# Optimization experiments

Hardware: AMD Instinct MI355X
Metric: run time of the kernel (lower is better)

The kernel has to match this reference:

```python
import jax, jax.numpy as jnp
import numpy as np

NUM_HEADS = 4
EPS = 1e-5


def setup_inputs() -> dict:
    key = jax.random.key(0)
    ks = jax.random.split(key, 5)
    B, C, H, W = 1, 128, 64, 64
    x = jax.random.normal(ks[0], (B, C, H, W), dtype=jnp.float32)
    # 1x1 conv weights [out_c, in_c]; scaled ~ kaiming-ish to keep softmax non-degenerate
    s = 1.0 / np.sqrt(C)
    qw = jax.random.normal(ks[1], (C, C), dtype=jnp.float32) * s
    kw = jax.random.normal(ks[2], (C, C), dtype=jnp.float32) * s
    vw = jax.random.normal(ks[3], (C, C), dtype=jnp.float32) * s
    pw = jax.random.normal(ks[4], (C, C), dtype=jnp.float32) * s
    zeros = jnp.zeros((C,), dtype=jnp.float32)
    return {
        "x": x,
        "gn_w": jnp.ones((C,), dtype=jnp.float32),
        "gn_b": zeros,
        "qw": qw, "qb": zeros,
        "kw": kw, "kb": zeros,
        "vw": vw, "vb": zeros,
        "pw": pw, "pb": zeros,
    }


def reference(x, gn_w, gn_b, qw, qb, kw, kb, vw, vb, pw, pb):
    B, C, H, W = x.shape
    N = H * W
    d = C // NUM_HEADS

    # GroupNorm(num_groups=1): normalize over (C,H,W) per sample, per-channel affine
    mean = jnp.mean(x, axis=(1, 2, 3), keepdims=True)
    var = jnp.var(x, axis=(1, 2, 3), keepdims=True)
    h = (x - mean) * jax.lax.rsqrt(var + EPS)
    h = h * gn_w[None, :, None, None] + gn_b[None, :, None, None]

    hf = h.reshape(B, C, N)  # [B,C,N]

    def conv1x1(w, b):  # 1x1 conv == channel GEMM
        return jnp.einsum('oc,bcn->bon', w, hf) + b[None, :, None]

    q = conv1x1(qw, qb).reshape(B, NUM_HEADS, d, N)
    k = conv1x1(kw, kb).reshape(B, NUM_HEADS, d, N)
    v = conv1x1(vw, vb).reshape(B, NUM_HEADS, d, N)

    scale = d ** (-0.5)
    attn = jnp.einsum('bhdn,bhdm->bhnm', q, k) * scale  # [B,H,N,N]
    attn = jax.nn.softmax(attn, axis=-1)
    out = jnp.einsum('bhnm,bhdm->bhdn', attn, v)  # [B,H,d,N]

    out = out.reshape(B, C, N)
    out = jnp.einsum('oc,bcn->bon', pw, out) + pb[None, :, None]
    return x + out.reshape(B, C, H, W)
```

## Files before the change

kernel.cpp:

```cpp
#include <hip/hip_runtime.h>

#define NPOS 4096
#define NCH  128
#define NTOT (NPOS * NCH)
#define NHEAD 4
#define DH    32
#define NSPLIT 4
#define KSPAN (NPOS / NSPLIT)
#define NTILE (KSPAN / 64)

typedef __attribute__((ext_vector_type(8))) short short8;
typedef __attribute__((ext_vector_type(4))) float floatx4;
typedef unsigned short u16;
typedef unsigned int   u32;

__device__ __forceinline__ u16 f2bf(float f) {
  u32 u = __float_as_uint(f);
  u += 0x7fffu + ((u >> 16) & 1u);
  return (u16)(u >> 16);
}
__device__ __forceinline__ u32 pack2bf(float a, float b) {
  return (u32)f2bf(a) | ((u32)f2bf(b) << 16);
}
__device__ __forceinline__ u32 pack2bf_fast(float a, float b) {
  return ((__float_as_uint(a) + 0x8000u) >> 16) |
         ((__float_as_uint(b) + 0x8000u) & 0xffff0000u);
}
__device__ __forceinline__ float bf2f(u16 h) {
  return __uint_as_float(((u32)h) << 16);
}

__global__ __launch_bounds__(256) void gn_prep_k(const float* __restrict__ x,
                                                 float2* __restrict__ partials,
                                                 u32* __restrict__ bounds,
                                                 const float* __restrict__ qw, const float* __restrict__ kw,
                                                 const float* __restrict__ vw, const float* __restrict__ pw,
                                                 u16* __restrict__ wq, u16* __restrict__ wk,
                                                 u16* __restrict__ wv, u16* __restrict__ wp) {
  int i = blockIdx.x * 256 + threadIdx.x;
  int w = threadIdx.x >> 6, lane = threadIdx.x & 63;
  float4 a = ((const float4*)x)[i];
  float s  = a.x + a.y + a.z + a.w;
  float sq = a.x*a.x + a.y*a.y + a.z*a.z + a.w*a.w;
#pragma unroll
  for (int m = 1; m < 64; m <<= 1) {
    s  += __shfl_xor(s, m);
    sq += __shfl_xor(sq, m);
  }
  __shared__ float red[8];
  if (lane == 0) { red[w] = s; red[4 + w] = sq; }
  __syncthreads();
  if (threadIdx.x == 0)
    partials[blockIdx.x] = make_float2(red[0]+red[1]+red[2]+red[3],
                                       red[4]+red[5]+red[6]+red[7]);
  if (blockIdx.x == 0 && threadIdx.x < 4) bounds[threadIdx.x] = 0;
  if (blockIdx.x < 16) {
    int t = blockIdx.x * 256 + threadIdx.x;
    const float sc = 0.17677669529663687f * 1.4426950408889634f;
    float4 v = ((const float4*)qw)[t];
    ((uint2*)wq)[t] = make_uint2(pack2bf(v.x*sc, v.y*sc), pack2bf(v.z*sc, v.w*sc));
    v = ((const float4*)kw)[t];
    ((uint2*)wk)[t] = make_uint2(pack2bf(v.x, v.y), pack2bf(v.z, v.w));
    v = ((const float4*)vw)[t];
    ((uint2*)wv)[t] = make_uint2(pack2bf(v.x, v.y), pack2bf(v.z, v.w));
    v = ((const float4*)pw)[t];
    ((uint2*)wp)[t] = make_uint2(pack2bf(v.x, v.y), pack2bf(v.z, v.w));
  }
}

__global__ __launch_bounds__(768) void qkv_k(const float* __restrict__ x,
    const float* __restrict__ gw, const float* __restrict__ gb,
    const float2* __restrict__ partials,
    const u16* __restrict__ wq, const u16* __restrict__ wk, const u16* __restrict__ wv,
    const float* __restrict__ qb, const float* __restrict__ kb, const float* __restrict__ vb,
    u16* __restrict__ q, u16* __restrict__ k, u16* __restrict__ v, u32* __restrict__ bounds) {
  const int t = threadIdx.x;
  const int w = t >> 6, lane = t & 63;
  const int l16 = lane & 15, quad = lane >> 4;
  const int n0 = blockIdx.x * 16;
  const floatx4 zero = {0.f, 0.f, 0.f, 0.f};

  __shared__ float red[16];
  __shared__ float2 swb[128];
  __shared__ __align__(16) u16 hs[16][136];

  if (t < 512) {
    float2 p = partials[t];
    float s = p.x, sq = p.y;
#pragma unroll
    for (int m = 1; m < 64; m <<= 1) {
      s  += __shfl_xor(s, m);
      sq += __shfl_xor(sq, m);
    }
    if (lane == 0) { red[w] = s; red[8 + w] = sq; }
  }
  __syncthreads();
  float mean = (red[0]+red[1]+red[2]+red[3]+red[4]+red[5]+red[6]+red[7]) * (1.0f / NTOT);
  float var  = (red[8]+red[9]+red[10]+red[11]+red[12]+red[13]+red[14]+red[15]) * (1.0f / NTOT)
               - mean * mean;
  float rstd = rsqrtf(var + 1e-5f);
  if (t < 128) {
    float swv = gw[t] * rstd;
    swb[t] = make_float2(swv, gb[t] - mean * swv);
  }
  __syncthreads();
  if (t < 512) {
    int c = t >> 2, seg = t & 3;
    float4 xv = *(const float4*)(x + (size_t)c * NPOS + n0 + seg * 4);
    float2 sb = swb[c];
    int nl = seg * 4;
    hs[nl + 0][c] = f2bf(xv.x * sb.x + sb.y);
    hs[nl + 1][c] = f2bf(xv.y * sb.x + sb.y);
    hs[nl + 2][c] = f2bf(xv.z * sb.x + sb.y);
    hs[nl + 3][c] = f2bf(xv.w * sb.x + sb.y);
  }
  __syncthreads();

  short8 bfr[4];
#pragma unroll
  for (int kk = 0; kk < 4; kk++)
    bfr[kk] = *(const short8*)&hs[l16][kk * 32 + quad * 8];

  const int mat = w >> 2, head = w & 3, ow = head * 32;
  const u16* wm = (mat == 0) ? wq : (mat == 1) ? wk : wv;
  floatx4 a0 = zero, a1 = zero;
  const u16* ap = wm + (size_t)(ow + l16) * NCH + quad * 8;
#pragma unroll
  for (int kk = 0; kk < 4; kk++) {
    a0 = __builtin_amdgcn_mfma_f32_16x16x32_bf16(*(const short8*)(ap + kk*32),          bfr[kk], a0, 0,0,0);
    a1 = __builtin_amdgcn_mfma_f32_16x16x32_bf16(*(const short8*)(ap + 16*NCH + kk*32), bfr[kk], a1, 0,0,0);
  }
  const int n = n0 + l16;
  if (mat == 0) {
    const float sc = 0.17677669529663687f * 1.4426950408889634f;
    u16* qp = q + (size_t)(head * NPOS + n) * DH;
#pragma unroll
    for (int ss = 0; ss < 2; ss++) {
      floatx4 acc = ss ? a1 : a0;
      int od = ss * 16 + quad * 4;
      float r0 = acc[0] + qb[ow+od+0]*sc, r1 = acc[1] + qb[ow+od+1]*sc;
      float r2 = acc[2] + qb[ow+od+2]*sc, r3 = acc[3] + qb[ow+od+3]*sc;
      *(uint2*)(qp + od) = make_uint2(pack2bf(r0, r1), pack2bf(r2, r3));
    }
  } else if (mat == 1) {
    float sumsq = 0.f;
    u16* kp = k + (size_t)(head * NPOS + n) * DH;
#pragma unroll
    for (int ss = 0; ss < 2; ss++) {
      floatx4 acc = ss ? a1 : a0;
      int od = ss * 16 + quad * 4;
      float r0 = acc[0] + kb[ow+od+0], r1 = acc[1] + kb[ow+od+1];
      float r2 = acc[2] + kb[ow+od+2], r3 = acc[3] + kb[ow+od+3];
      sumsq += r0*r0 + r1*r1 + r2*r2 + r3*r3;
      *(uint2*)(kp + od) = make_uint2(pack2bf(r0, r1), pack2bf(r2, r3));
    }
    sumsq += __shfl_xor(sumsq, 16);
    sumsq += __shfl_xor(sumsq, 32);
#pragma unroll
    for (int m = 1; m < 16; m <<= 1) sumsq = fmaxf(sumsq, __shfl_xor(sumsq, m));
    if (lane == 0) atomicMax(&bounds[head], __float_as_uint(sumsq));
  } else {
    u16* vp = v + (size_t)(head * DH) * NPOS + n;
#pragma unroll
    for (int ss = 0; ss < 2; ss++) {
      floatx4 acc = ss ? a1 : a0;
      int od = ss * 16 + quad * 4;
#pragma unroll
      for (int r = 0; r < 4; r++)
        vp[(size_t)(od + r) * NPOS] = f2bf(acc[r] + vb[ow + od + r]);
    }
  }
}

__global__ __launch_bounds__(256) void attn_k(const u16* __restrict__ q, const u16* __restrict__ k,
                                              const u16* __restrict__ v, const u32* __restrict__ bounds,
                                              u32* __restrict__ Opair, float* __restrict__ lpart) {
  const int w = threadIdx.x >> 6, lane = threadIdx.x & 63;
  const int l16 = lane & 15, quad = lane >> 4;
  const int s = blockIdx.x >> 8;
  const int q0 = (blockIdx.x & 255) * 16;
  const int head = w;
  __shared__ __align__(16) u16 p_lds[4][2][16][72];

  short8 bq = *(const short8*)(q + (size_t)(head * NPOS + q0 + l16) * DH + quad * 8);
  float qn2 = 0.f;
#pragma unroll
  for (int j = 0; j < 8; j++) { float f = bf2f((u16)bq[j]); qn2 += f * f; }
  qn2 += __shfl_xor(qn2, 16);
  qn2 += __shfl_xor(qn2, 32);
  float kmax = sqrtf(__uint_as_float(bounds[head])) * 1.0005f;
  float bound = sqrtf(qn2) * kmax;

  floatx4 o0 = {0,0,0,0}, o1 = {0,0,0,0}, ol = {0,0,0,0};
  short8 ones;
#pragma unroll
  for (int j = 0; j < 8; j++) ones[j] = (short)0x3F80;

  const u16* kbp = k + (size_t)head * NPOS * DH + quad * 8;
  const u16* vb0 = v + (size_t)(head * DH + l16) * NPOS + quad * 8;
  const u16* vb1 = vb0 + (size_t)16 * NPOS;
  const floatx4 zero = {0,0,0,0};

  int m0 = s * KSPAN;
  short8 ak[4], av[4];
#pragma unroll
  for (int sub = 0; sub < 4; sub++)
    ak[sub] = *(const short8*)(kbp + (size_t)(m0 + sub * 16 + l16) * DH);
#pragma unroll
  for (int kc = 0; kc < 2; kc++) {
    av[2*kc]   = *(const short8*)(vb0 + m0 + kc * 32);
    av[2*kc+1] = *(const short8*)(vb1 + m0 + kc * 32);
  }

  for (int it = 0; it < NTILE; it++) {
    const int mn = m0 + 64;
    const bool more = (it + 1 < NTILE);
    short8 nak[4], nav[4];
    if (more) {
#pragma unroll
      for (int sub = 0; sub < 4; sub++)
        nak[sub] = *(const short8*)(kbp + (size_t)(mn + sub * 16 + l16) * DH);
#pragma unroll
      for (int kc = 0; kc < 2; kc++) {
        nav[2*kc]   = *(const short8*)(vb0 + mn + kc * 32);
        nav[2*kc+1] = *(const short8*)(vb1 + mn + kc * 32);
      }
    }
    const int buf = it & 1;
    floatx4 c[4];
#pragma unroll
    for (int sub = 0; sub < 4; sub++)
      c[sub] = __builtin_amdgcn_mfma_f32_16x16x32_bf16(ak[sub], bq, zero, 0, 0, 0);
#pragma unroll
    for (int sub = 0; sub < 4; sub++) {
      float p0 = __builtin_amdgcn_exp2f(c[sub][0] - bound);
      float p1 = __builtin_amdgcn_exp2f(c[sub][1] - bound);
      float p2 = __builtin_amdgcn_exp2f(c[sub][2] - bound);
      float p3 = __builtin_amdgcn_exp2f(c[sub][3] - bound);
      *(uint2*)&p_lds[w][buf][l16][sub * 16 + quad * 4] =
          make_uint2(pack2bf_fast(p0, p1), pack2bf_fast(p2, p3));
    }
#pragma unroll
    for (int kc = 0; kc < 2; kc++) {
      short8 pa = *(const short8*)&p_lds[w][buf][l16][kc * 32 + quad * 8];
      o0 = __builtin_amdgcn_mfma_f32_16x16x32_bf16(pa, av[2*kc],   o0, 0, 0, 0);
      o1 = __builtin_amdgcn_mfma_f32_16x16x32_bf16(pa, av[2*kc+1], o1, 0, 0, 0);
      ol = __builtin_amdgcn_mfma_f32_16x16x32_bf16(pa, ones,       ol, 0, 0, 0);
    }
    if (more) {
#pragma unroll
      for (int j = 0; j < 4; j++) { ak[j] = nak[j]; av[j] = nav[j]; }
    }
    m0 = mn;
  }

  u32*   op = Opair + (size_t)(s * NHEAD + head) * NPOS * 16;
  float* lp = lpart + (size_t)(s * NHEAD + head) * NPOS;
#pragma unroll
  for (int r = 0; r < 4; r++) {
    int qq = q0 + quad * 4 + r;
    op[(size_t)qq * 16 + l16] = pack2bf(o0[r], o1[r]);
    if (l16 == 0) lp[qq] = ol[r];
  }
}

__global__ __launch_bounds__(512) void proj_k(const u32* __restrict__ Opair,
                                              const float* __restrict__ lpart,
                                              const u16* __restrict__ wp,
                                              const float* __restrict__ pb,
                                              const float* __restrict__ x,
                                              float* __restrict__ out) {
  const int t = threadIdx.x;
  const int w = t >> 6, lane = t & 63;
  const int l16 = lane & 15, quad = lane >> 4;
  const int n0 = blockIdx.x * 16;
  const floatx4 zero = {0.f, 0.f, 0.f, 0.f};
  __shared__ __align__(16) u16 at_lds[16][136];

  {
    const int n = t & 15, ci = t >> 4;
    const int c0 = ci * 4, head = c0 >> 5, off = c0 & 31;
    const int half = off >> 4, j0 = off & 15;
    float acc[4] = {0.f, 0.f, 0.f, 0.f};
    float l = 0.f;
#pragma unroll
    for (int s2 = 0; s2 < NSPLIT; s2++) {
      const u32* pp = Opair + ((size_t)(s2 * NHEAD + head) * NPOS + n0 + n) * 16 + j0;
      uint4 u = *(const uint4*)pp;
      u32 uu[4] = {u.x, u.y, u.z, u.w};
#pragma unroll
      for (int j = 0; j < 4; j++)
        acc[j] += half ? __uint_as_float(uu[j] & 0xffff0000u)
                       : __uint_as_float(uu[j] << 16);
      l += lpart[(size_t)(s2 * NHEAD + head) * NPOS + n0 + n];
    }
    float inv = 1.0f / fmaxf(l, 1e-30f);
    *(uint2*)&at_lds[n][c0] = make_uint2(pack2bf(acc[0]*inv, acc[1]*inv),
                                         pack2bf(acc[2]*inv, acc[3]*inv));
  }
  __syncthreads();

  short8 bfr[4];
#pragma unroll
  for (int kk = 0; kk < 4; kk++)
    bfr[kk] = *(const short8*)&at_lds[l16][kk * 32 + quad * 8];
  const int ow = w * 16;
  floatx4 a0 = zero;
  const u16* ap = wp + (size_t)(ow + l16) * NCH + quad * 8;
#pragma unroll
  for (int kk = 0; kk < 4; kk++)
    a0 = __builtin_amdgcn_mfma_f32_16x16x32_bf16(*(const short8*)(ap + kk*32), bfr[kk], a0, 0,0,0);
  const int n = n0 + l16;
#pragma unroll
  for (int r = 0; r < 4; r++) {
    int o = ow + quad * 4 + r;
    size_t idx = (size_t)o * NPOS + n;
    out[idx] = a0[r] + pb[o] + x[idx];
  }
}

extern "C" void kernel_launch(void* const* d_in, const int* in_sizes, int n_in,
                              void* d_out, int out_size, void* d_ws, size_t ws_size,
                              hipStream_t stream) {
  const float* x   = (const float*)d_in[0];
  const float* gnw = (const float*)d_in[1];
  const float* gnb = (const float*)d_in[2];
  const float* qw  = (const float*)d_in[3];
  const float* qb  = (const float*)d_in[4];
  const float* kw  = (const float*)d_in[5];
  const float* kb  = (const float*)d_in[6];
  const float* vw  = (const float*)d_in[7];
  const float* vb  = (const float*)d_in[8];
  const float* pw  = (const float*)d_in[9];
  const float* pb  = (const float*)d_in[10];
  float* out = (float*)d_out;

  char* wsb = (char*)d_ws;
  float2* partials = (float2*)wsb;
  u32*    bounds   = (u32*)(wsb + 4096);
  u16* wqb = (u16*)(wsb + 8192);
  u16* wkb = wqb + 16384;
  u16* wvb = wkb + 16384;
  u16* wpb = wvb + 16384;
  u16* qbuf = wpb + 16384;
  u16* kbuf = qbuf + NTOT;
  u16* vbuf = kbuf + NTOT;
  u32* Opair = (u32*)(vbuf + NTOT);
  float* lpart = (float*)(Opair + (size_t)NSPLIT * NHEAD * NPOS * 16);

  gn_prep_k<<<512, 256, 0, stream>>>(x, partials, bounds, qw, kw, vw, pw,
                                     wqb, wkb, wvb, wpb);
  qkv_k<<<256, 768, 0, stream>>>(x, gnw, gnb, partials, wqb, wkb, wvb,
                                 qb, kb, vb, qbuf, kbuf, vbuf, bounds);
  attn_k<<<256 * NSPLIT, 256, 0, stream>>>(qbuf, kbuf, vbuf, bounds, Opair, lpart);
  proj_k<<<256, 512, 0, stream>>>(Opair, lpart, wpb, pb, x, out);
}
```

Before: 144.5 us.

## Permute key rows so QK MFMA output feeds PV MFMA directly from registers

Reorders which key positions each lane loads for the QK^T MFMA so the accumulator layout matches the A-operand layout needed by the P·V MFMA. The probabilities are exponentiated and packed in registers instead of round-tripping through a shared-memory P buffer, which removes LDS stores, loads and the associated waits. Correctness relies on the permuted key index mapping staying consistent with the V columns consumed per k-chunk.

```diff
diff --git a/kernel.cpp b/kernel.cpp
--- a/kernel.cpp
+++ b/kernel.cpp
@@ -180,7 +180,6 @@
   const int s = blockIdx.x >> 8;
   const int q0 = (blockIdx.x & 255) * 16;
   const int head = w;
-  __shared__ __align__(16) u16 p_lds[4][2][16][72];
 
   short8 bq = *(const short8*)(q + (size_t)(head * NPOS + q0 + l16) * DH + quad * 8);
   float qn2 = 0.f;
@@ -196,6 +195,11 @@
 #pragma unroll
   for (int j = 0; j < 8; j++) ones[j] = (short)0x3F80;
 
+  int ko[4];
+#pragma unroll
+  for (int s2 = 0; s2 < 4; s2++)
+    ko[s2] = 32 * (s2 >> 1) + (l16 >> 2) * 8 + (s2 & 1) * 4 + (l16 & 3);
+
   const u16* kbp = k + (size_t)head * NPOS * DH + quad * 8;
   const u16* vb0 = v + (size_t)(head * DH + l16) * NPOS + quad * 8;
   const u16* vb1 = vb0 + (size_t)16 * NPOS;
@@ -204,8 +208,8 @@
   int m0 = s * KSPAN;
   short8 ak[4], av[4];
 #pragma unroll
-  for (int sub = 0; sub < 4; sub++)
-    ak[sub] = *(const short8*)(kbp + (size_t)(m0 + sub * 16 + l16) * DH);
+  for (int s2 = 0; s2 < 4; s2++)
+    ak[s2] = *(const short8*)(kbp + (size_t)(m0 + ko[s2]) * DH);
 #pragma unroll
   for (int kc = 0; kc < 2; kc++) {
     av[2*kc]   = *(const short8*)(vb0 + m0 + kc * 32);
@@ -218,31 +222,31 @@
     short8 nak[4], nav[4];
     if (more) {
 #pragma unroll
-      for (int sub = 0; sub < 4; sub++)
-        nak[sub] = *(const short8*)(kbp + (size_t)(mn + sub * 16 + l16) * DH);
+      for (int s2 = 0; s2 < 4; s2++)
+        nak[s2] = *(const short8*)(kbp + (size_t)(mn + ko[s2]) * DH);
 #pragma unroll
       for (int kc = 0; kc < 2; kc++) {
         nav[2*kc]   = *(const short8*)(vb0 + mn + kc * 32);
         nav[2*kc+1] = *(const short8*)(vb1 + mn + kc * 32);
       }
     }
-    const int buf = it & 1;
     floatx4 c[4];
 #pragma unroll
-    for (int sub = 0; sub < 4; sub++)
-      c[sub] = __builtin_amdgcn_mfma_f32_16x16x32_bf16(ak[sub], bq, zero, 0, 0, 0);
-#pragma unroll
-    for (int sub = 0; sub < 4; sub++) {
-      float p0 = __builtin_amdgcn_exp2f(c[sub][0] - bound);
-      float p1 = __builtin_amdgcn_exp2f(c[sub][1] - bound);
-      float p2 = __builtin_amdgcn_exp2f(c[sub][2] - bound);
-      float p3 = __builtin_amdgcn_exp2f(c[sub][3] - bound);
-      *(uint2*)&p_lds[w][buf][l16][sub * 16 + quad * 4] =
-          make_uint2(pack2bf_fast(p0, p1), pack2bf_fast(p2, p3));
-    }
+    for (int s2 = 0; s2 < 4; s2++)
+      c[s2] = __builtin_amdgcn_mfma_f32_16x16x32_bf16(ak[s2], bq, zero, 0, 0, 0);
 #pragma unroll
     for (int kc = 0; kc < 2; kc++) {
-      short8 pa = *(const short8*)&p_lds[w][buf][l16][kc * 32 + quad * 8];
+      float pa0 = __builtin_amdgcn_exp2f(c[2*kc][0] - bound);
+      float pa1 = __builtin_amdgcn_exp2f(c[2*kc][1] - bound);
+      float pa2 = __builtin_amdgcn_exp2f(c[2*kc][2] - bound);
+      float pa3 = __builtin_amdgcn_exp2f(c[2*kc][3] - bound);
+      float pb0 = __builtin_amdgcn_exp2f(c[2*kc+1][0] - bound);
+      float pb1 = __builtin_amdgcn_exp2f(c[2*kc+1][1] - bound);
+      float pb2 = __builtin_amdgcn_exp2f(c[2*kc+1][2] - bound);
+      float pb3 = __builtin_amdgcn_exp2f(c[2*kc+1][3] - bound);
+      uint4 uu = make_uint4(pack2bf_fast(pa0, pa1), pack2bf_fast(pa2, pa3),
+                            pack2bf_fast(pb0, pb1), pack2bf_fast(pb2, pb3));
+      short8 pa = *(short8*)&uu;
       o0 = __builtin_amdgcn_mfma_f32_16x16x32_bf16(pa, av[2*kc],   o0, 0, 0, 0);
       o1 = __builtin_amdgcn_mfma_f32_16x16x32_bf16(pa, av[2*kc+1], o1, 0, 0, 0);
       ol = __builtin_amdgcn_mfma_f32_16x16x32_bf16(pa, ones,       ol, 0, 0, 0);
```

Result: no change. 145.5 us (+0.7%).

## Register-block four query tiles per wave and drop the LDS round trip for P

Applied to the files above, without the earlier changes.

Each wave now processes 64 queries as four 16-row fragments, so every K/V fragment it loads feeds four times as many MFMAs. K rows are loaded in a permuted order so the QK^T MFMA output can be packed straight into the A operand of the PV MFMA, which removes the shared-memory store and reload of P. The softmax bound is folded into the MFMA accumulator init, the key range is split eight ways instead of four, and K/V loads are double-buffered in registers. The costs are higher register pressure (hinted with launch_bounds 256,2) and twice as many partial outputs for the projection kernel to combine.

```diff
diff --git a/kernel.cpp b/kernel.cpp
--- a/kernel.cpp
+++ b/kernel.cpp
@@ -5,7 +5,7 @@
 #define NTOT (NPOS * NCH)
 #define NHEAD 4
 #define DH    32
-#define NSPLIT 4
+#define NSPLIT 8
 #define KSPAN (NPOS / NSPLIT)
 #define NTILE (KSPAN / 64)
 
@@ -172,95 +172,117 @@
   }
 }
 
-__global__ __launch_bounds__(256) void attn_k(const u16* __restrict__ q, const u16* __restrict__ k,
-                                              const u16* __restrict__ v, const u32* __restrict__ bounds,
-                                              u32* __restrict__ Opair, float* __restrict__ lpart) {
+__global__ __launch_bounds__(256, 2) void attn_k(const u16* __restrict__ q, const u16* __restrict__ k,
+                                                 const u16* __restrict__ v, const u32* __restrict__ bounds,
+                                                 u32* __restrict__ Opair, float* __restrict__ lpart) {
   const int w = threadIdx.x >> 6, lane = threadIdx.x & 63;
   const int l16 = lane & 15, quad = lane >> 4;
-  const int s = blockIdx.x >> 8;
-  const int q0 = (blockIdx.x & 255) * 16;
+  const int s = blockIdx.x >> 6;
+  const int q0w = (blockIdx.x & 63) * 64;
   const int head = w;
-  __shared__ __align__(16) u16 p_lds[4][2][16][72];
-
-  short8 bq = *(const short8*)(q + (size_t)(head * NPOS + q0 + l16) * DH + quad * 8);
-  float qn2 = 0.f;
-#pragma unroll
-  for (int j = 0; j < 8; j++) { float f = bf2f((u16)bq[j]); qn2 += f * f; }
-  qn2 += __shfl_xor(qn2, 16);
-  qn2 += __shfl_xor(qn2, 32);
+
   float kmax = sqrtf(__uint_as_float(bounds[head])) * 1.0005f;
-  float bound = sqrtf(qn2) * kmax;
-
-  floatx4 o0 = {0,0,0,0}, o1 = {0,0,0,0}, ol = {0,0,0,0};
+
+  short8 bq[4];
+  floatx4 cb[4];
+#pragma unroll
+  for (int qf = 0; qf < 4; qf++) {
+    bq[qf] = *(const short8*)(q + (size_t)(head * NPOS + q0w + qf * 16 + l16) * DH + quad * 8);
+    float qn2 = 0.f;
+#pragma unroll
+    for (int j = 0; j < 8; j++) { float f = bf2f((u16)bq[qf][j]); qn2 += f * f; }
+    qn2 += __shfl_xor(qn2, 16);
+    qn2 += __shfl_xor(qn2, 32);
+    float nb = -sqrtf(qn2) * kmax;
+    cb[qf][0] = nb; cb[qf][1] = nb; cb[qf][2] = nb; cb[qf][3] = nb;
+  }
+
+  floatx4 o0[4], o1[4], ol[4];
+#pragma unroll
+  for (int qf = 0; qf < 4; qf++) {
+    o0[qf] = (floatx4){0,0,0,0}; o1[qf] = (floatx4){0,0,0,0}; ol[qf] = (floatx4){0,0,0,0};
+  }
   short8 ones;
 #pragma unroll
   for (int j = 0; j < 8; j++) ones[j] = (short)0x3F80;
 
-  const u16* kbp = k + (size_t)head * NPOS * DH + quad * 8;
-  const u16* vb0 = v + (size_t)(head * DH + l16) * NPOS + quad * 8;
-  const u16* vb1 = vb0 + (size_t)16 * NPOS;
-  const floatx4 zero = {0,0,0,0};
-
-  int m0 = s * KSPAN;
-  short8 ak[4], av[4];
-#pragma unroll
-  for (int sub = 0; sub < 4; sub++)
-    ak[sub] = *(const short8*)(kbp + (size_t)(m0 + sub * 16 + l16) * DH);
-#pragma unroll
-  for (int kc = 0; kc < 2; kc++) {
-    av[2*kc]   = *(const short8*)(vb0 + m0 + kc * 32);
-    av[2*kc+1] = *(const short8*)(vb1 + m0 + kc * 32);
-  }
-
+  const int ko0 = (l16 >> 2) * 8 + (l16 & 3);
+  const u16* kbase  = k + (size_t)head * NPOS * DH + (size_t)(s * KSPAN + ko0) * DH + quad * 8;
+  const u16* vbase0 = v + (size_t)(head * DH + l16) * NPOS + s * KSPAN + quad * 8;
+  const u16* vbase1 = vbase0 + (size_t)16 * NPOS;
+
+  short8 akA[4], avA[4], akB[4], avB[4];
+
+  auto loadT = [&](short8* ak, short8* av, int it) {
+    const u16* kb = kbase + it * 2048;
+    ak[0] = *(const short8*)(kb);
+    ak[1] = *(const short8*)(kb + 128);
+    ak[2] = *(const short8*)(kb + 1024);
+    ak[3] = *(const short8*)(kb + 1152);
+    const u16* v0 = vbase0 + it * 64;
+    const u16* v1 = vbase1 + it * 64;
+    av[0] = *(const short8*)(v0);
+    av[1] = *(const short8*)(v1);
+    av[2] = *(const short8*)(v0 + 32);
+    av[3] = *(const short8*)(v1 + 32);
+  };
+
+  auto compute = [&](const short8* ak, const short8* av) {
+#pragma unroll
+    for (int qf = 0; qf < 4; qf++) {
+      floatx4 c0 = __builtin_amdgcn_mfma_f32_16x16x32_bf16(ak[0], bq[qf], cb[qf], 0, 0, 0);
+      floatx4 c1 = __builtin_amdgcn_mfma_f32_16x16x32_bf16(ak[1], bq[qf], cb[qf], 0, 0, 0);
+      floatx4 c2 = __builtin_amdgcn_mfma_f32_16x16x32_bf16(ak[2], bq[qf], cb[qf], 0, 0, 0);
+      floatx4 c3 = __builtin_amdgcn_mfma_f32_16x16x32_bf16(ak[3], bq[qf], cb[qf], 0, 0, 0);
+      {
+        float p0 = __builtin_amdgcn_exp2f(c0[0]), p1 = __builtin_amdgcn_exp2f(c0[1]);
+        float p2 = __builtin_amdgcn_exp2f(c0[2]), p3 = __builtin_amdgcn_exp2f(c0[3]);
+        float p4 = __builtin_amdgcn_exp2f(c1[0]), p5 = __builtin_amdgcn_exp2f(c1[1]);
+        float p6 = __builtin_amdgcn_exp2f(c1[2]), p7 = __builtin_amdgcn_exp2f(c1[3]);
+        uint4 uu = make_uint4(pack2bf_fast(p0, p1), pack2bf_fast(p2, p3),
+                              pack2bf_fast(p4, p5), pack2bf_fast(p6, p7));
+        short8 pa = *(short8*)&uu;
+        o0[qf] = __builtin_amdgcn_mfma_f32_16x16x32_bf16(pa, av[0], o0[qf], 0, 0, 0);
+        o1[qf] = __builtin_amdgcn_mfma_f32_16x16x32_bf16(pa, av[1], o1[qf], 0, 0, 0);
+        ol[qf] = __builtin_amdgcn_mfma_f32_16x16x32_bf16(pa, ones,  ol[qf], 0, 0, 0);
+      }
+      {
+        float p0 = __builtin_amdgcn_exp2f(c2[0]), p1 = __builtin_amdgcn_exp2f(c2[1]);
+        float p2 = __builtin_amdgcn_exp2f(c2[2]), p3 = __builtin_amdgcn_exp2f(c2[3]);
+        float p4 = __builtin_amdgcn_exp2f(c3[0]), p5 = __builtin_amdgcn_exp2f(c3[1]);
+        float p6 = __builtin_amdgcn_exp2f(c3[2]), p7 = __builtin_amdgcn_exp2f(c3[3]);
+        uint4 uu = make_uint4(pack2bf_fast(p0, p1), pack2bf_fast(p2, p3),
+                              pack2bf_fast(p4, p5), pack2bf_fast(p6, p7));
+        short8 pa = *(short8*)&uu;
+        o0[qf] = __builtin_amdgcn_mfma_f32_16x16x32_bf16(pa, av[2], o0[qf], 0, 0, 0);
+        o1[qf] = __builtin_amdgcn_mfma_f32_16x16x32_bf16(pa, av[3], o1[qf], 0, 0, 0);
+        ol[qf] = __builtin_amdgcn_mfma_f32_16x16x32_bf16(pa, ones,  ol[qf], 0, 0, 0);
+      }
+    }
+  };
+
+  loadT(akA, avA, 0);
+#pragma unroll
   for (int it = 0; it < NTILE; it++) {
-    const int mn = m0 + 64;
-    const bool more = (it + 1 < NTILE);
-    short8 nak[4], nav[4];
-    if (more) {
-#pragma unroll
-      for (int sub = 0; sub < 4; sub++)
-        nak[sub] = *(const short8*)(kbp + (size_t)(mn + sub * 16 + l16) * DH);
-#pragma unroll
-      for (int kc = 0; kc < 2; kc++) {
-        nav[2*kc]   = *(const short8*)(vb0 + mn + kc * 32);
-        nav[2*kc+1] = *(const short8*)(vb1 + mn + kc * 32);
-      }
-    }
-    const int buf = it & 1;
-    floatx4 c[4];
-#pragma unroll
-    for (int sub = 0; sub < 4; sub++)
-      c[sub] = __builtin_amdgcn_mfma_f32_16x16x32_bf16(ak[sub], bq, zero, 0, 0, 0);
-#pragma unroll
-    for (int sub = 0; sub < 4; sub++) {
-      float p0 = __builtin_amdgcn_exp2f(c[sub][0] - bound);
-      float p1 = __builtin_amdgcn_exp2f(c[sub][1] - bound);
-      float p2 = __builtin_amdgcn_exp2f(c[sub][2] - bound);
-      float p3 = __builtin_amdgcn_exp2f(c[sub][3] - bound);
-      *(uint2*)&p_lds[w][buf][l16][sub * 16 + quad * 4] =
-          make_uint2(pack2bf_fast(p0, p1), pack2bf_fast(p2, p3));
-    }
-#pragma unroll
-    for (int kc = 0; kc < 2; kc++) {
-      short8 pa = *(const short8*)&p_lds[w][buf][l16][kc * 32 + quad * 8];
-      o0 = __builtin_amdgcn_mfma_f32_16x16x32_bf16(pa, av[2*kc],   o0, 0, 0, 0);
-      o1 = __builtin_amdgcn_mfma_f32_16x16x32_bf16(pa, av[2*kc+1], o1, 0, 0, 0);
-      ol = __builtin_amdgcn_mfma_f32_16x16x32_bf16(pa, ones,       ol, 0, 0, 0);
-    }
-    if (more) {
-#pragma unroll
-      for (int j = 0; j < 4; j++) { ak[j] = nak[j]; av[j] = nav[j]; }
-    }
-    m0 = mn;
+    if ((it & 1) == 0) {
+      if (it + 1 < NTILE) loadT(akB, avB, it + 1);
+      compute(akA, avA);
+    } else {
+      if (it + 1 < NTILE) loadT(akA, avA, it + 1);
+      compute(akB, avB);
+    }
   }
 
   u32*   op = Opair + (size_t)(s * NHEAD + head) * NPOS * 16;
   float* lp = lpart + (size_t)(s * NHEAD + head) * NPOS;
 #pragma unroll
-  for (int r = 0; r < 4; r++) {
-    int qq = q0 + quad * 4 + r;
-    op[(size_t)qq * 16 + l16] = pack2bf(o0[r], o1[r]);
-    if (l16 == 0) lp[qq] = ol[r];
+  for (int qf = 0; qf < 4; qf++) {
+#pragma unroll
+    for (int r = 0; r < 4; r++) {
+      int qq = q0w + qf * 16 + quad * 4 + r;
+      op[(size_t)qq * 16 + l16] = pack2bf(o0[qf][r], o1[qf][r]);
+      if (l16 == 0) lp[qq] = ol[qf][r];
+    }
   }
 }
 
@@ -352,6 +374,6 @@
                                      wqb, wkb, wvb, wpb);
   qkv_k<<<256, 768, 0, stream>>>(x, gnw, gnb, partials, wqb, wkb, wvb,
                                  qb, kb, vb, qbuf, kbuf, vbuf, bounds);
-  attn_k<<<256 * NSPLIT, 256, 0, stream>>>(qbuf, kbuf, vbuf, bounds, Opair, lpart);
+  attn_k<<<64 * NSPLIT, 256, 0, stream>>>(qbuf, kbuf, vbuf, bounds, Opair, lpart);
   proj_k<<<256, 512, 0, stream>>>(Opair, lpart, wpb, pb, x, out);
 }
```

New measurement: 117.8 us. 1.23x faster.
